# Kernel tuning notes

Hardware: AMD Instinct MI355X
Metric: run time of the kernel (lower is better)

Reference implementation:

```python
import jax, jax.numpy as jnp
import numpy as np

RC = 5.2                                   # radial cutoff Rcr
ETA_R = np.array([16.0], dtype=np.float32)
SHF_R = (0.9 + 0.26875 * np.arange(16)).astype(np.float32)
NUM_SPECIES = 4                             # len(vocabulary)


def setup_inputs() -> dict:
    key = jax.random.key(0)
    kp, ks = jax.random.split(key)
    B, N = 64, 256
    # random positions in a 12 A box -> realistic distance matrices
    pos = jax.random.uniform(kp, (B, N, 3), jnp.float32, 0.0, 12.0)
    diff = pos[:, :, None, :] - pos[:, None, :, :]
    d = jnp.sqrt(jnp.sum(diff * diff, axis=-1) + 1e-12)
    d = d * (1.0 - jnp.eye(N, dtype=jnp.float32))  # zero self-distance
    species = jax.random.randint(ks, (B, N), 1, NUM_SPECIES + 1, jnp.int32)
    return {"distance_matrices_batch": d, "num_species_batch": species}


def reference(distance_matrices_batch, num_species_batch):
    d = distance_matrices_batch                      # [B, N, N]
    eta = jnp.asarray(ETA_R)
    shf = jnp.asarray(SHF_R)
    # cartesian product of (EtaR, ShfR), P = len(EtaR)*len(ShfR)
    eta_p = jnp.repeat(eta, shf.shape[0])            # [P]
    shf_p = jnp.tile(shf, eta.shape[0])              # [P]

    mask = (d < RC) & (d != 0.0)                     # [B, N, N]
    fc = 0.5 * jnp.cos(jnp.pi * d / RC) + 0.5        # ANAKIN cutoff fn
    # Gaussian radial terms, masked to the cutoff neighborhood
    terms = jnp.exp(-eta_p * (d[..., None] - shf_p) ** 2) * fc[..., None]  # [B,N,N,P]
    terms = jnp.where(mask[..., None], terms, jnp.zeros((), terms.dtype))

    # one-hot of neighbor species (IDs are 1-based)
    oh = jax.nn.one_hot(num_species_batch - 1, NUM_SPECIES, dtype=terms.dtype)  # [B,N,S]
    # scatter-sum over neighbors j, bucketed by species of j
    GR = jnp.einsum('bijp,bjs->bisp', terms, oh)     # [B, N, S, P]
    B, N = d.shape[0], d.shape[1]
    return GR.reshape(B, N, NUM_SPECIES * terms.shape[-1])  # [B, N, S*P]
```

## Files before the change

### kernel.cpp

```cpp
#include <hip/hip_runtime.h>
#include <stdint.h>


static __device__ __forceinline__ int mbcnt64(uint64_t m) {
    int lo = __builtin_amdgcn_mbcnt_lo((uint32_t)m, 0u);
    return __builtin_amdgcn_mbcnt_hi((uint32_t)(m >> 32), lo);
}

__global__ __launch_bounds__(256) void aev_kernel(
    const float* __restrict__ dmat,
    const int* __restrict__ species,
    float* __restrict__ out)
{
    __shared__ alignas(16) int pos[256];
    __shared__ float2 comp[4][260];
    __shared__ int    cntm[4][4];

    const int tid  = threadIdx.x;
    const int w    = tid >> 6;
    const int lane = tid & 63;
    const int blk  = (int)blockIdx.x;
    const int row  = blk * 4 + w;
    const int b    = blk >> 6;

    const float4* rp = (const float4*)(dmat + ((size_t)row << 8));
    const float4 q4 = rp[lane];

    int sj = species[(b << 8) + tid] - 1;
    sj = (sj < 0) ? 0 : ((sj > 3) ? 3 : sj);
    const uint64_t bs0 = __ballot((sj & 1) != 0);
    const uint64_t bs1 = __ballot((sj & 2) != 0);
    const uint64_t m0 = ~bs0 & ~bs1, m1 = bs0 & ~bs1;
    const uint64_t m2 = ~bs0 &  bs1, m3 = bs0 &  bs1;
    if (lane == 0) {
        cntm[w][0] = __popcll(m0); cntm[w][1] = __popcll(m1);
        cntm[w][2] = __popcll(m2); cntm[w][3] = __popcll(m3);
    }
    uint64_t msel = m0;
    msel = (sj == 1) ? m1 : msel;
    msel = (sj == 2) ? m2 : msel;
    msel = (sj == 3) ? m3 : msel;
    const int rank = mbcnt64(msel);
    __syncthreads();

    int seg[5];
    seg[0] = 0;
    int base = 0;
    #pragma unroll
    for (int s = 0; s < 4; ++s) {
        const int t4 = cntm[0][s] + cntm[1][s] + cntm[2][s] + cntm[3][s];
        base += (s < sj) ? t4 : 0;
        seg[s + 1] = seg[s] + t4;
    }
    #pragma unroll
    for (int w2 = 0; w2 < 3; ++w2) base += (w2 < w) ? cntm[w2][sj] : 0;
    pos[tid] = base + rank;
    __syncthreads();

    {
        const int4 p4 = *(const int4*)&pos[4 * lane];
        const float dv[4] = {q4.x, q4.y, q4.z, q4.w};
        const int   pp[4] = {p4.x, p4.y, p4.z, p4.w};
        #pragma unroll
        for (int e = 0; e < 4; ++e) {
            const float dd = dv[e];
            const bool  v  = (dd < 5.2f) && (dd != 0.0f);
            const float x  = v ? dd : 2.6f;
            const float fc = 0.5f * __builtin_amdgcn_cosf(x * (0.5f / 5.2f)) + 0.5f;
            comp[w][pp[e]] = make_float2(x, v ? fc : 0.0f);
        }
    }
    __syncthreads();

    const int p = lane >> 2;
    const int q = lane & 3;
    const float shfp = 0.9f + 0.26875f * (float)p;
    float accs[4];
    #pragma unroll
    for (int s = 0; s < 4; ++s) {
        float a = 0.0f;
        for (int k = seg[s] + q; k < seg[s + 1]; k += 4) {
            const float2 dw = comp[w][k];
            const float u = dw.x - shfp;
            const float t = __builtin_amdgcn_exp2f(u * u * -23.083120654223414f);
            a = __builtin_fmaf(t, dw.y, a);
        }
        accs[s] = a;
    }
    #pragma unroll
    for (int s = 0; s < 4; ++s) {
        accs[s] += __shfl_xor(accs[s], 1, 64);
        accs[s] += __shfl_xor(accs[s], 2, 64);
    }
    float vout = accs[0];
    vout = (q == 1) ? accs[1] : vout;
    vout = (q == 2) ? accs[2] : vout;
    vout = (q == 3) ? accs[3] : vout;
    __builtin_nontemporal_store(vout, &out[((size_t)row << 6) + (size_t)((q << 4) + p)]);
}

extern "C" void kernel_launch(void* const* d_in, const int* in_sizes, int n_in,
                              void* d_out, int out_size, void* d_ws, size_t ws_size,
                              hipStream_t stream) {
    const float* dmat  = (const float*)d_in[0];
    const int* species = (const int*)d_in[1];
    float* o           = (float*)d_out;
    const int B = in_sizes[1] >> 8;
    aev_kernel<<<dim3(B * 64), 256, 0, stream>>>(dmat, species, o);
}
```

Baseline: 79.13 us.

## Process two rows per wave with padded species segments and float4 LDS reads

Each wave now handles two distance-matrix rows, so the species sort and compaction setup is shared across eight rows per block and the grid is halved. Species segments are padded to multiples of eight and pre-filled with zero-weight entries. This allows branch-free float4 LDS loads that process two neighbours per row per iteration. The cost is extra padded exp work, more LDS per block, and a zero-fill pass.

```diff
diff --git a/kernel.cpp b/kernel.cpp
--- a/kernel.cpp
+++ b/kernel.cpp
@@ -12,19 +12,19 @@
     const int* __restrict__ species,
     float* __restrict__ out)
 {
+    __shared__ alignas(16) float2 comp[8][288];
     __shared__ alignas(16) int pos[256];
-    __shared__ float2 comp[4][260];
-    __shared__ int    cntm[4][4];
+    __shared__ int cntm[4][4];
 
     const int tid  = threadIdx.x;
     const int w    = tid >> 6;
     const int lane = tid & 63;
     const int blk  = (int)blockIdx.x;
-    const int row  = blk * 4 + w;
-    const int b    = blk >> 6;
+    const int row0 = blk * 8 + w * 2;
+    const int b    = blk >> 5;
 
-    const float4* rp = (const float4*)(dmat + ((size_t)row << 8));
-    const float4 q4 = rp[lane];
+    const float4 qa = ((const float4*)(dmat + ((size_t)row0 << 8)))[lane];
+    const float4 qb = ((const float4*)(dmat + ((size_t)(row0 + 1) << 8)))[lane];
 
     int sj = species[(b << 8) + tid] - 1;
     sj = (sj < 0) ? 0 : ((sj > 3) ? 3 : sj);
@@ -41,33 +41,57 @@
     msel = (sj == 2) ? m2 : msel;
     msel = (sj == 3) ? m3 : msel;
     const int rank = mbcnt64(msel);
+
+    {
+        float2* cz = &comp[0][0];
+        #pragma unroll
+        for (int k = 0; k < 9; ++k) cz[tid + 256 * k] = make_float2(2.6f, 0.0f);
+    }
     __syncthreads();
 
-    int seg[5];
-    seg[0] = 0;
-    int base = 0;
+    int segP[5], nIt[4];
+    segP[0] = 0;
     #pragma unroll
     for (int s = 0; s < 4; ++s) {
-        const int t4 = cntm[0][s] + cntm[1][s] + cntm[2][s] + cntm[3][s];
-        base += (s < sj) ? t4 : 0;
-        seg[s + 1] = seg[s] + t4;
+        const int t4  = cntm[0][s] + cntm[1][s] + cntm[2][s] + cntm[3][s];
+        const int t4p = (t4 + 7) & ~7;
+        nIt[s]     = t4p >> 3;
+        segP[s + 1] = segP[s] + t4p;
     }
-    #pragma unroll
-    for (int w2 = 0; w2 < 3; ++w2) base += (w2 < w) ? cntm[w2][sj] : 0;
-    pos[tid] = base + rank;
+    {
+        int base = segP[0];
+        base = (sj == 1) ? segP[1] : base;
+        base = (sj == 2) ? segP[2] : base;
+        base = (sj == 3) ? segP[3] : base;
+        int wadd = 0;
+        #pragma unroll
+        for (int w2 = 0; w2 < 3; ++w2) wadd += (w2 < w) ? cntm[w2][sj] : 0;
+        const int slot = base + wadd + rank;
+        pos[tid] = (slot < 287) ? slot : 287;
+    }
     __syncthreads();
 
     {
         const int4 p4 = *(const int4*)&pos[4 * lane];
-        const float dv[4] = {q4.x, q4.y, q4.z, q4.w};
         const int   pp[4] = {p4.x, p4.y, p4.z, p4.w};
+        const float da[4] = {qa.x, qa.y, qa.z, qa.w};
+        const float db[4] = {qb.x, qb.y, qb.z, qb.w};
+        const int lr = w * 2;
         #pragma unroll
         for (int e = 0; e < 4; ++e) {
-            const float dd = dv[e];
+            const float dd = da[e];
             const bool  v  = (dd < 5.2f) && (dd != 0.0f);
             const float x  = v ? dd : 2.6f;
             const float fc = 0.5f * __builtin_amdgcn_cosf(x * (0.5f / 5.2f)) + 0.5f;
-            comp[w][pp[e]] = make_float2(x, v ? fc : 0.0f);
+            comp[lr][pp[e]] = make_float2(x, v ? fc : 0.0f);
+        }
+        #pragma unroll
+        for (int e = 0; e < 4; ++e) {
+            const float dd = db[e];
+            const bool  v  = (dd < 5.2f) && (dd != 0.0f);
+            const float x  = v ? dd : 2.6f;
+            const float fc = 0.5f * __builtin_amdgcn_cosf(x * (0.5f / 5.2f)) + 0.5f;
+            comp[lr + 1][pp[e]] = make_float2(x, v ? fc : 0.0f);
         }
     }
     __syncthreads();
@@ -75,28 +99,41 @@
     const int p = lane >> 2;
     const int q = lane & 3;
     const float shfp = 0.9f + 0.26875f * (float)p;
-    float accs[4];
+    const int lr = w * 2;
+    float acc[2][4];
     #pragma unroll
     for (int s = 0; s < 4; ++s) {
-        float a = 0.0f;
-        for (int k = seg[s] + q; k < seg[s + 1]; k += 4) {
-            const float2 dw = comp[w][k];
-            const float u = dw.x - shfp;
-            const float t = __builtin_amdgcn_exp2f(u * u * -23.083120654223414f);
-            a = __builtin_fmaf(t, dw.y, a);
+        float a0 = 0.0f, a1 = 0.0f;
+        const int k0 = segP[s] + 2 * q;
+        const int n  = nIt[s];
+        for (int m = 0; m < n; ++m) {
+            const int k = k0 + 8 * m;
+            const float4 f0 = *(const float4*)&comp[lr][k];
+            const float4 f1 = *(const float4*)&comp[lr + 1][k];
+            float u;
+            u = f0.x - shfp; a0 = __builtin_fmaf(__builtin_amdgcn_exp2f(u * u * -23.083120654223414f), f0.y, a0);
+            u = f0.z - shfp; a0 = __builtin_fmaf(__builtin_amdgcn_exp2f(u * u * -23.083120654223414f), f0.w, a0);
+            u = f1.x - shfp; a1 = __builtin_fmaf(__builtin_amdgcn_exp2f(u * u * -23.083120654223414f), f1.y, a1);
+            u = f1.z - shfp; a1 = __builtin_fmaf(__builtin_amdgcn_exp2f(u * u * -23.083120654223414f), f1.w, a1);
         }
-        accs[s] = a;
+        acc[0][s] = a0; acc[1][s] = a1;
     }
     #pragma unroll
-    for (int s = 0; s < 4; ++s) {
-        accs[s] += __shfl_xor(accs[s], 1, 64);
-        accs[s] += __shfl_xor(accs[s], 2, 64);
+    for (int rr = 0; rr < 2; ++rr)
+        #pragma unroll
+        for (int s = 0; s < 4; ++s) {
+            acc[rr][s] += __shfl_xor(acc[rr][s], 1, 64);
+            acc[rr][s] += __shfl_xor(acc[rr][s], 2, 64);
+        }
+    #pragma unroll
+    for (int rr = 0; rr < 2; ++rr) {
+        float vout = acc[rr][0];
+        vout = (q == 1) ? acc[rr][1] : vout;
+        vout = (q == 2) ? acc[rr][2] : vout;
+        vout = (q == 3) ? acc[rr][3] : vout;
+        __builtin_nontemporal_store(vout,
+            &out[((size_t)(row0 + rr) << 6) + (size_t)((q << 4) + p)]);
     }
-    float vout = accs[0];
-    vout = (q == 1) ? accs[1] : vout;
-    vout = (q == 2) ? accs[2] : vout;
-    vout = (q == 3) ? accs[3] : vout;
-    __builtin_nontemporal_store(vout, &out[((size_t)row << 6) + (size_t)((q << 4) + p)]);
 }
 
 extern "C" void kernel_launch(void* const* d_in, const int* in_sizes, int n_in,
@@ -106,5 +143,5 @@
     const int* species = (const int*)d_in[1];
     float* o           = (float*)d_out;
     const int B = in_sizes[1] >> 8;
-    aev_kernel<<<dim3(B * 64), 256, 0, stream>>>(dmat, species, o);
+    aev_kernel<<<dim3(B * 32), 256, 0, stream>>>(dmat, species, o);
 }
```

Result: no change. 79.66 us (+0.7%).
